# Performance work log

Measured on AMD Instinct MI355X. Metric: run time of the kernel, lower is better.

The kernel has to match this reference:

```python
import jax, jax.numpy as jnp
import numpy as np

B, T, V, D, H, L = 64, 256, 65, 384, 6, 6
HD = D // H
FF = 4 * D
EPS = 1e-5


def _layernorm(x, w, b):
    m = x.mean(-1, keepdims=True)
    v = ((x - m) ** 2).mean(-1, keepdims=True)
    return (x - m) / jnp.sqrt(v + EPS) * w + b


def setup_inputs() -> dict:
    key = jax.random.key(0)
    ks = jax.random.split(key, 20)
    s = lambda k, shape, scale=0.02: jax.random.normal(k, shape, dtype=jnp.float32) * scale
    inp = {
        'idx': jax.random.randint(ks[0], (B, T), 0, V),
        'tok_emb': s(ks[1], (V, D)),
        'pos_emb': s(ks[2], (T, D)),
        'ln1_w': jnp.ones((L, D), jnp.float32),
        'ln1_b': jnp.zeros((L, D), jnp.float32),
        'wq': s(ks[3], (L, H, D, HD)),
        'wk': s(ks[4], (L, H, D, HD)),
        'wv': s(ks[5], (L, H, D, HD)),
        'proj_w': s(ks[6], (L, D, D)),
        'proj_b': jnp.zeros((L, D), jnp.float32),
        'ln2_w': jnp.ones((L, D), jnp.float32),
        'ln2_b': jnp.zeros((L, D), jnp.float32),
        'ff_w1': s(ks[7], (L, D, FF)),
        'ff_b1': jnp.zeros((L, FF), jnp.float32),
        'ff_w2': s(ks[8], (L, FF, D)),
        'ff_b2': jnp.zeros((L, D), jnp.float32),
        'lnf_w': jnp.ones((D,), jnp.float32),
        'lnf_b': jnp.zeros((D,), jnp.float32),
        'head_w': s(ks[9], (D, V)),
        'head_b': jnp.zeros((V,), jnp.float32),
    }
    return inp


def reference(idx, tok_emb, pos_emb, ln1_w, ln1_b, wq, wk, wv, proj_w, proj_b,
              ln2_w, ln2_b, ff_w1, ff_b1, ff_w2, ff_b2, lnf_w, lnf_b, head_w, head_b):
    t = idx.shape[1]
    x = tok_emb[idx] + pos_emb[:t]  # [B,T,D]
    causal = jnp.tril(jnp.ones((t, t), bool))
    scale = D ** -0.5  # NOTE: original scales by n_embd**-0.5, not head_size
    for l in range(L):
        h = _layernorm(x, ln1_w[l], ln1_b[l])
        q = jnp.einsum('btd,hde->bhte', h, wq[l])
        k = jnp.einsum('btd,hde->bhte', h, wk[l])
        v = jnp.einsum('btd,hde->bhte', h, wv[l])
        wei = jnp.einsum('bhte,bhse->bhts', q, k) * scale
        wei = jnp.where(causal, wei, -jnp.inf)
        wei = jax.nn.softmax(wei, axis=-1)
        o = jnp.einsum('bhts,bhse->bhte', wei, v)
        o = o.transpose(0, 2, 1, 3).reshape(x.shape[0], t, D)  # concat heads
        x = x + o @ proj_w[l] + proj_b[l]
        h2 = _layernorm(x, ln2_w[l], ln2_b[l])
        x = x + jnp.maximum(h2 @ ff_w1[l] + ff_b1[l], 0.0) @ ff_w2[l] + ff_b2[l]
    x = _layernorm(x, lnf_w, lnf_b)
    logits = x @ head_w + head_b  # [B,T,V]
    return logits
```

## Files before the change

### kernel.cpp

```cpp
#include <hip/hip_runtime.h>
#include <hip/hip_bf16.h>
#include <math.h>

#define BB   64
#define TT   256
#define VV   65
#define DD   384
#define HH   6
#define HDD  64
#define LL   6
#define FFD  1536
#define BT   (BB * TT)
#define EPSL 1e-5f
#define SCALE 0.05103103630798287f

using bf16x8 = __attribute__((ext_vector_type(8))) short;
using f32x4  = __attribute__((ext_vector_type(4))) float;

__device__ __forceinline__ short f2bf(float f) {
    __hip_bfloat16 h = __float2bfloat16(f);
    return *reinterpret_cast<short*>(&h);
}

__device__ __forceinline__ void load_lds16(const void* g, void* lds_base) {
    __builtin_amdgcn_global_load_lds(
        (const __attribute__((address_space(1))) void*)g,
        (__attribute__((address_space(3))) void*)lds_base,
        16, 0, 0);
}

__global__ __launch_bounds__(256) void embed_k(const int* __restrict__ idx,
                                               const float* __restrict__ tok,
                                               const float* __restrict__ pos,
                                               float* __restrict__ x) {
    int i = blockIdx.x * 256 + threadIdx.x;
    int bt = i / 96;
    int d4 = i - bt * 96;
    int t  = bt & (TT - 1);
    float4 a = ((const float4*)tok)[(size_t)idx[bt] * 96 + d4];
    float4 p = ((const float4*)pos)[(size_t)t * 96 + d4];
    float4 o;
    o.x = a.x + p.x; o.y = a.y + p.y; o.z = a.z + p.z; o.w = a.w + p.w;
    ((float4*)x)[i] = o;
}

__global__ __launch_bounds__(256) void ln_k(const float* __restrict__ in,
                                            const float* __restrict__ w,
                                            const float* __restrict__ b,
                                            short* __restrict__ out) {
    int row  = blockIdx.x * 4 + (threadIdx.x >> 6);
    int lane = threadIdx.x & 63;
    const float* p = in + (size_t)row * DD;
    float vals[6];
    float s = 0.f;
#pragma unroll
    for (int j = 0; j < 6; ++j) { vals[j] = p[lane + 64 * j]; s += vals[j]; }
#pragma unroll
    for (int off = 32; off; off >>= 1) s += __shfl_xor(s, off);
    float mean = s * (1.0f / DD);
    float s2 = 0.f;
#pragma unroll
    for (int j = 0; j < 6; ++j) { float d = vals[j] - mean; s2 += d * d; }
#pragma unroll
    for (int off = 32; off; off >>= 1) s2 += __shfl_xor(s2, off);
    float rstd = rsqrtf(s2 * (1.0f / DD) + EPSL);
    short* po = out + (size_t)row * DD;
#pragma unroll
    for (int j = 0; j < 6; ++j) {
        int c = lane + 64 * j;
        po[c] = f2bf((vals[j] - mean) * rstd * w[c] + b[c]);
    }
}

__global__ __launch_bounds__(256) void wconv_k(const float* __restrict__ W,
                                               short* __restrict__ Wt,
                                               int K, int N, int Npad) {
    __shared__ float tile[32][33];
    W  += (size_t)blockIdx.z * K * N;
    Wt += (size_t)blockIdx.z * Npad * K;
    const int t  = threadIdx.x;
    const int c  = t & 31;
    const int r8 = t >> 5;
    const int k0 = blockIdx.y * 32;
    const int n0 = blockIdx.x * 32;
#pragma unroll
    for (int p = 0; p < 4; ++p) {
        int kk = r8 + 8 * p;
        int n  = n0 + c;
        tile[kk][c] = (n < N) ? W[(size_t)(k0 + kk) * N + n] : 0.f;
    }
    __syncthreads();
#pragma unroll
    for (int p = 0; p < 4; ++p) {
        int nl = r8 + 8 * p;
        Wt[(size_t)(n0 + nl) * K + k0 + c] = f2bf(tile[c][nl]);
    }
}

__global__ __launch_bounds__(256) void qkvconv_k(const float* __restrict__ wq,
                                                 const float* __restrict__ wk,
                                                 const float* __restrict__ wv,
                                                 short* __restrict__ Wt) {
    int tid = blockIdx.x * 256 + threadIdx.x;
    int e  = tid & 63;
    int k  = (tid >> 6) % 384;
    int r2 = (tid >> 6) / 384;
    int h  = r2 % 6;
    int r3 = r2 / 6;
    int part = r3 % 3;
    int l  = r3 / 3;
    const float* src = (part == 0) ? wq : (part == 1) ? wk : wv;
    float v = src[(((size_t)l * 6 + h) * 384 + k) * 64 + e];
    Wt[((size_t)l * 1152 + part * 384 + h * 64 + e) * 384 + k] = f2bf(v);
}

__global__ __launch_bounds__(256, 8) void gemm64_k(
    const short* __restrict__ A,
    const short* __restrict__ Bt,
    const float* __restrict__ bias,
    const float* __restrict__ res,
    float* __restrict__ out32,
    short* __restrict__ out16,
    int M, int K, int ldC, int ld16, int Nmax, int relu) {
    __shared__ short As[4096];
    __shared__ short Bs[4096];
    const int t  = threadIdx.x;
    const int w  = t >> 6;
    const int l  = t & 63;

    const int gx  = gridDim.x;
    const int nwg = gx * gridDim.y;
    const int lin = blockIdx.y * gx + blockIdx.x;
    const int cpx = nwg >> 3;
    const int swz = (lin & 7) * cpx + (lin >> 3);
    const int m0 = (swz / gx) * 64;
    const int n0 = (swz % gx) * 64;

    const int wr = w >> 1, wc = w & 1;
    const int fr = l & 15, fq = l >> 4;

    int srow[2], scol[2];
#pragma unroll
    for (int qi = 0; qi < 2; ++qi) {
        int s = w * 2 + qi;
        int r = s * 8 + (l >> 3);
        int c = l & 7;
        srow[qi] = r;
        scol[qi] = c ^ (r & 7);
    }

    f32x4 acc[2][2];
#pragma unroll
    for (int i = 0; i < 2; ++i)
#pragma unroll
        for (int j = 0; j < 2; ++j) acc[i][j] = (f32x4)(0.0f);

    const int nt = K >> 6;

    for (int tk = 0; tk < nt; ++tk) {
        const int k0 = tk << 6;
#pragma unroll
        for (int qi = 0; qi < 2; ++qi) {
            load_lds16(A + (size_t)(m0 + srow[qi]) * K + k0 + scol[qi] * 8,
                       (char*)As + (w * 2 + qi) * 1024);
        }
#pragma unroll
        for (int qi = 0; qi < 2; ++qi) {
            load_lds16(Bt + (size_t)(n0 + srow[qi]) * K + k0 + scol[qi] * 8,
                       (char*)Bs + (w * 2 + qi) * 1024);
        }
        asm volatile("s_waitcnt vmcnt(0)" ::: "memory");
        __syncthreads();

        __builtin_amdgcn_s_setprio(1);
#pragma unroll
        for (int ks = 0; ks < 2; ++ks) {
            const int kc = ks * 4 + fq;
            bf16x8 af[2], bfv[2];
#pragma unroll
            for (int mf = 0; mf < 2; ++mf) {
                int ar = wr * 32 + mf * 16 + fr;
                af[mf] = *reinterpret_cast<const bf16x8*>(
                    (const char*)As + ar * 128 + ((kc ^ (ar & 7)) << 4));
            }
#pragma unroll
            for (int nf = 0; nf < 2; ++nf) {
                int br = wc * 32 + nf * 16 + fr;
                bfv[nf] = *reinterpret_cast<const bf16x8*>(
                    (const char*)Bs + br * 128 + ((kc ^ (br & 7)) << 4));
            }
#pragma unroll
            for (int mf = 0; mf < 2; ++mf)
#pragma unroll
                for (int nf = 0; nf < 2; ++nf)
                    acc[mf][nf] = __builtin_amdgcn_mfma_f32_16x16x32_bf16(
                        af[mf], bfv[nf], acc[mf][nf], 0, 0, 0);
        }
        __builtin_amdgcn_s_setprio(0);
        __syncthreads();
    }

#pragma unroll
    for (int mf = 0; mf < 2; ++mf) {
#pragma unroll
        for (int nf = 0; nf < 2; ++nf) {
            int n = n0 + wc * 32 + nf * 16 + fr;
            if (n < Nmax) {
#pragma unroll
                for (int j = 0; j < 4; ++j) {
                    int m = m0 + wr * 32 + mf * 16 + fq * 4 + j;
                    float v = acc[mf][nf][j];
                    if (bias)  v += bias[n];
                    if (res)   v += res[(size_t)m * ldC + n];
                    if (relu)  v = fmaxf(v, 0.f);
                    if (out32) out32[(size_t)m * ldC + n] = v;
                    if (out16) out16[(size_t)m * ld16 + n] = f2bf(v);
                }
            }
        }
    }
}

__global__ __launch_bounds__(256) void attn_mfma_k(const short* __restrict__ qkv,
                                                   short* __restrict__ o) {
    __shared__ short Vt[16384];
    __shared__ short Pw[4][4096];

    const int hh = blockIdx.x;
    const int bb = blockIdx.y;
    const int t  = threadIdx.x;
    const int w  = t >> 6;
    const int lane = t & 63;
    const int fr = lane & 15, fq = lane >> 4;
    const int bt0 = bb * TT;

    {
        const int r0 = (t & 127) * 2;
        const int dbase = (t >> 7) * 32;
        const short* v0 = qkv + (size_t)(bt0 + r0) * 1152 + 768 + hh * 64 + dbase;
        short a0[32], a1[32];
#pragma unroll
        for (int i = 0; i < 4; ++i) {
            *(bf16x8*)(a0 + i * 8) = *(const bf16x8*)(v0 + i * 8);
            *(bf16x8*)(a1 + i * 8) = *(const bf16x8*)(v0 + 1152 + i * 8);
        }
#pragma unroll
        for (int i = 0; i < 32; ++i) {
            int d = dbase + i;
            int byte = (d * 512 + r0 * 2) ^ ((d & 7) << 4);
            unsigned int pk = (unsigned int)(unsigned short)a0[i] |
                              ((unsigned int)(unsigned short)a1[i] << 16);
            *(unsigned int*)((char*)Vt + byte) = pk;
        }
    }
    __syncthreads();

    char* PwW = (char*)Pw[w];

    bf16x8 qb[4][2];
#pragma unroll
    for (int nf = 0; nf < 4; ++nf)
#pragma unroll
        for (int ks = 0; ks < 2; ++ks)
            qb[nf][ks] = *(const bf16x8*)(qkv + (size_t)(bt0 + w * 64 + nf * 16 + fr) * 1152 +
                                          hh * 64 + ks * 32 + fq * 8);

    f32x4 o_acc[4][4];
#pragma unroll
    for (int i = 0; i < 4; ++i)
#pragma unroll
        for (int j = 0; j < 4; ++j) o_acc[i][j] = (f32x4)(0.0f);
    float m_run[4], l_run[4];
#pragma unroll
    for (int nf = 0; nf < 4; ++nf) { m_run[nf] = -1e30f; l_run[nf] = 0.f; }

    for (int kt = 0; kt <= w; ++kt) {
        bf16x8 ak[4][2];
#pragma unroll
        for (int mf = 0; mf < 4; ++mf)
#pragma unroll
            for (int ks = 0; ks < 2; ++ks)
                ak[mf][ks] = *(const bf16x8*)(qkv + (size_t)(bt0 + kt * 64 + mf * 16 + fr) * 1152 +
                                              384 + hh * 64 + ks * 32 + fq * 8);

        f32x4 s[4][4];
#pragma unroll
        for (int i = 0; i < 4; ++i)
#pragma unroll
            for (int j = 0; j < 4; ++j) s[i][j] = (f32x4)(0.0f);
#pragma unroll
        for (int ks = 0; ks < 2; ++ks)
#pragma unroll
            for (int mf = 0; mf < 4; ++mf)
#pragma unroll
                for (int nf = 0; nf < 4; ++nf)
                    s[mf][nf] = __builtin_amdgcn_mfma_f32_16x16x32_bf16(
                        ak[mf][ks], qb[nf][ks], s[mf][nf], 0, 0, 0);

        const bool diag = (kt == w);
#pragma unroll
        for (int mf = 0; mf < 4; ++mf)
#pragma unroll
            for (int nf = 0; nf < 4; ++nf)
#pragma unroll
                for (int j = 0; j < 4; ++j) {
                    float v = s[mf][nf][j] * SCALE;
                    if (diag && (mf * 16 + fq * 4 + j > nf * 16 + fr)) v = -1e30f;
                    s[mf][nf][j] = v;
                }

        float fac[4];
#pragma unroll
        for (int nf = 0; nf < 4; ++nf) {
            float mx = -1e30f;
#pragma unroll
            for (int mf = 0; mf < 4; ++mf)
#pragma unroll
                for (int j = 0; j < 4; ++j) mx = fmaxf(mx, s[mf][nf][j]);
            mx = fmaxf(mx, __shfl_xor(mx, 16));
            mx = fmaxf(mx, __shfl_xor(mx, 32));
            float mnew = fmaxf(m_run[nf], mx);
            fac[nf] = __expf(m_run[nf] - mnew);
            m_run[nf] = mnew;
        }

#pragma unroll
        for (int nf = 0; nf < 4; ++nf) {
            float ps = 0.f;
#pragma unroll
            for (int mf = 0; mf < 4; ++mf)
#pragma unroll
                for (int j = 0; j < 4; ++j) {
                    float p = __expf(s[mf][nf][j] - m_run[nf]);
                    s[mf][nf][j] = p;
                    ps += p;
                }
            ps += __shfl_xor(ps, 16);
            ps += __shfl_xor(ps, 32);
            l_run[nf] = l_run[nf] * fac[nf] + ps;
        }

#pragma unroll
        for (int mf = 0; mf < 4; ++mf)
#pragma unroll
            for (int nf = 0; nf < 4; ++nf) {
                unsigned long long pk =
                    (unsigned long long)(unsigned short)f2bf(s[mf][nf][0]) |
                    ((unsigned long long)(unsigned short)f2bf(s[mf][nf][1]) << 16) |
                    ((unsigned long long)(unsigned short)f2bf(s[mf][nf][2]) << 32) |
                    ((unsigned long long)(unsigned short)f2bf(s[mf][nf][3]) << 48);
                int q = nf * 16 + fr;
                int byte = (q * 128 + mf * 32 + fq * 8) ^ ((q & 7) << 4);
                *(unsigned long long*)(PwW + byte) = pk;
            }

#pragma unroll
        for (int j = 0; j < 4; ++j) {
            int src = (lane & 48) + ((lane & 48) >> 2) + j;
#pragma unroll
            for (int mo = 0; mo < 4; ++mo) {
                float f = __shfl(fac[mo], src);
#pragma unroll
                for (int df = 0; df < 4; ++df) o_acc[mo][df][j] *= f;
            }
        }

        bf16x8 ap[4][2], bv[4][2];
#pragma unroll
        for (int mo = 0; mo < 4; ++mo)
#pragma unroll
            for (int ks = 0; ks < 2; ++ks) {
                int byte = ((mo * 16 + fr) * 128 + ks * 64 + fq * 16) ^ ((fr & 7) << 4);
                ap[mo][ks] = *(const bf16x8*)(PwW + byte);
            }
#pragma unroll
        for (int df = 0; df < 4; ++df)
#pragma unroll
            for (int ks = 0; ks < 2; ++ks) {
                int byte = ((df * 16 + fr) * 512 + kt * 128 + ks * 64 + fq * 16) ^ ((fr & 7) << 4);
                bv[df][ks] = *(const bf16x8*)((const char*)Vt + byte);
            }
#pragma unroll
        for (int ks = 0; ks < 2; ++ks)
#pragma unroll
            for (int mo = 0; mo < 4; ++mo)
#pragma unroll
                for (int df = 0; df < 4; ++df)
                    o_acc[mo][df] = __builtin_amdgcn_mfma_f32_16x16x32_bf16(
                        ap[mo][ks], bv[df][ks], o_acc[mo][df], 0, 0, 0);
    }

    float linv[4];
#pragma unroll
    for (int nf = 0; nf < 4; ++nf) linv[nf] = 1.0f / l_run[nf];
#pragma unroll
    for (int j = 0; j < 4; ++j) {
        int src = (lane & 48) + ((lane & 48) >> 2) + j;
#pragma unroll
        for (int mo = 0; mo < 4; ++mo) {
            float li = __shfl(linv[mo], src);
#pragma unroll
            for (int df = 0; df < 4; ++df) {
                float val = o_acc[mo][df][j] * li;
                o[(size_t)(bt0 + w * 64 + mo * 16 + fq * 4 + j) * DD + hh * 64 + df * 16 + fr] =
                    f2bf(val);
            }
        }
    }
}

extern "C" void kernel_launch(void* const* d_in, const int* in_sizes, int n_in,
                              void* d_out, int out_size, void* d_ws, size_t ws_size,
                              hipStream_t stream) {
    const int*   idx     = (const int*)d_in[0];
    const float* tok_emb = (const float*)d_in[1];
    const float* pos_emb = (const float*)d_in[2];
    const float* ln1_w   = (const float*)d_in[3];
    const float* ln1_b   = (const float*)d_in[4];
    const float* wq      = (const float*)d_in[5];
    const float* wk      = (const float*)d_in[6];
    const float* wv      = (const float*)d_in[7];
    const float* proj_w  = (const float*)d_in[8];
    const float* proj_b  = (const float*)d_in[9];
    const float* ln2_w   = (const float*)d_in[10];
    const float* ln2_b   = (const float*)d_in[11];
    const float* ff_w1   = (const float*)d_in[12];
    const float* ff_b1   = (const float*)d_in[13];
    const float* ff_w2   = (const float*)d_in[14];
    const float* ff_b2   = (const float*)d_in[15];
    const float* lnf_w   = (const float*)d_in[16];
    const float* lnf_b   = (const float*)d_in[17];
    const float* head_w  = (const float*)d_in[18];
    const float* head_b  = (const float*)d_in[19];
    float* out = (float*)d_out;

    char* p = (char*)d_ws;
    float* x      = (float*)p;  p += (size_t)BT * DD * 4;
    short* qkv16  = (short*)p;  p += (size_t)BT * 1152 * 2;
    short* h16    = (short*)p;  p += (size_t)BT * DD * 2;
    short* o16    = (short*)p;  p += (size_t)BT * DD * 2;
    short* ff16   = (short*)p;  p += (size_t)BT * FFD * 2;
    short* wqkvT  = (short*)p;  p += (size_t)LL * 1152 * 384 * 2;
    short* projT  = (short*)p;  p += (size_t)LL * 384 * 384 * 2;
    short* ff1T   = (short*)p;  p += (size_t)LL * 1536 * 384 * 2;
    short* ff2T   = (short*)p;  p += (size_t)LL * 384 * 1536 * 2;
    short* headT  = (short*)p;  p += (size_t)128 * 384 * 2;

    const dim3 blk(256);

    qkvconv_k<<<dim3(2654208 / 256), blk, 0, stream>>>(wq, wk, wv, wqkvT);
    wconv_k<<<dim3(12, 12, 6), blk, 0, stream>>>(proj_w, projT, 384, 384, 384);
    wconv_k<<<dim3(48, 12, 6), blk, 0, stream>>>(ff_w1, ff1T, 384, 1536, 1536);
    wconv_k<<<dim3(12, 48, 6), blk, 0, stream>>>(ff_w2, ff2T, 1536, 384, 384);
    wconv_k<<<dim3(4, 12, 1), blk, 0, stream>>>(head_w, headT, 384, 65, 128);

    embed_k<<<dim3((BT * 96) / 256), blk, 0, stream>>>(idx, tok_emb, pos_emb, x);

    const dim3 gLN(BT / 4);
    const dim3 gAttn(HH, BB);
    const dim3 gQKV(1152 / 64, BT / 64);
    const dim3 gD(384 / 64, BT / 64);
    const dim3 gFF(1536 / 64, BT / 64);
    const dim3 gHead(128 / 64, BT / 64);

    for (int l = 0; l < LL; ++l) {
        const size_t dOff = (size_t)l * DD;

        ln_k<<<gLN, blk, 0, stream>>>(x, ln1_w + dOff, ln1_b + dOff, h16);

        gemm64_k<<<gQKV, blk, 0, stream>>>(h16, wqkvT + (size_t)l * 1152 * 384,
                                           nullptr, nullptr, nullptr, qkv16,
                                           BT, 384, 1152, 1152, 1152, 0);

        attn_mfma_k<<<gAttn, blk, 0, stream>>>(qkv16, o16);

        gemm64_k<<<gD, blk, 0, stream>>>(o16, projT + (size_t)l * 384 * 384,
                                         proj_b + dOff, x, x, nullptr,
                                         BT, 384, 384, 0, 384, 0);

        ln_k<<<gLN, blk, 0, stream>>>(x, ln2_w + dOff, ln2_b + dOff, h16);

        gemm64_k<<<gFF, blk, 0, stream>>>(h16, ff1T + (size_t)l * 1536 * 384,
                                          ff_b1 + (size_t)l * FFD, nullptr,
                                          nullptr, ff16,
                                          BT, 384, 1536, 1536, 1536, 1);

        gemm64_k<<<gD, blk, 0, stream>>>(ff16, ff2T + (size_t)l * 384 * 1536,
                                         ff_b2 + dOff, x, x, nullptr,
                                         BT, 1536, 384, 0, 384, 0);
    }

    ln_k<<<gLN, blk, 0, stream>>>(x, lnf_w, lnf_b, h16);
    gemm64_k<<<gHead, blk, 0, stream>>>(h16, headT, head_b, nullptr, out, nullptr,
                                        BT, 384, 65, 0, 65, 0);
}
```

Before: 1.195 ms.

## Store residual stream in bf16 and enlarge GEMM tiles to 128x64

The residual activation x is now kept in bf16 instead of fp32: embedding, layernorm input and the GEMM residual epilogue all read and write bf16, which halves that memory traffic. The GEMM kernel moves from 64x64 to 128x64 output tiles with 4x2 MFMA fragments per wave, so each B tile is reused more and fewer blocks are launched. The cost is that the residual accumulates rounding error in bf16 across layers, plus higher register and LDS use per block, which lowers occupancy.

```diff
diff --git a/kernel.cpp b/kernel.cpp
--- a/kernel.cpp
+++ b/kernel.cpp
@@ -21,6 +21,11 @@
     __hip_bfloat16 h = __float2bfloat16(f);
     return *reinterpret_cast<short*>(&h);
 }
+__device__ __forceinline__ float bf2f(short s) {
+    union { unsigned u; float f; } c;
+    c.u = ((unsigned)(unsigned short)s) << 16;
+    return c.f;
+}
 
 __device__ __forceinline__ void load_lds16(const void* g, void* lds_base) {
     __builtin_amdgcn_global_load_lds(
@@ -32,44 +37,52 @@
 __global__ __launch_bounds__(256) void embed_k(const int* __restrict__ idx,
                                                const float* __restrict__ tok,
                                                const float* __restrict__ pos,
-                                               float* __restrict__ x) {
+                                               short* __restrict__ x) {
     int i = blockIdx.x * 256 + threadIdx.x;
-    int bt = i / 96;
-    int d4 = i - bt * 96;
+    int bt = i / 48;
+    int g  = i - bt * 48;
     int t  = bt & (TT - 1);
-    float4 a = ((const float4*)tok)[(size_t)idx[bt] * 96 + d4];
-    float4 p = ((const float4*)pos)[(size_t)t * 96 + d4];
-    float4 o;
-    o.x = a.x + p.x; o.y = a.y + p.y; o.z = a.z + p.z; o.w = a.w + p.w;
-    ((float4*)x)[i] = o;
-}
-
-__global__ __launch_bounds__(256) void ln_k(const float* __restrict__ in,
+    const float4* tp = (const float4*)tok + (size_t)idx[bt] * 96 + g * 2;
+    const float4* pp = (const float4*)pos + (size_t)t * 96 + g * 2;
+    float4 a0 = tp[0], a1 = tp[1], p0 = pp[0], p1 = pp[1];
+    bf16x8 o;
+    o[0] = f2bf(a0.x + p0.x); o[1] = f2bf(a0.y + p0.y);
+    o[2] = f2bf(a0.z + p0.z); o[3] = f2bf(a0.w + p0.w);
+    o[4] = f2bf(a1.x + p1.x); o[5] = f2bf(a1.y + p1.y);
+    o[6] = f2bf(a1.z + p1.z); o[7] = f2bf(a1.w + p1.w);
+    *reinterpret_cast<bf16x8*>(x + (size_t)bt * DD + g * 8) = o;
+}
+
+__global__ __launch_bounds__(256) void ln_k(const short* __restrict__ in,
                                             const float* __restrict__ w,
                                             const float* __restrict__ b,
                                             short* __restrict__ out) {
     int row  = blockIdx.x * 4 + (threadIdx.x >> 6);
     int lane = threadIdx.x & 63;
-    const float* p = in + (size_t)row * DD;
-    float vals[6];
-    float s = 0.f;
-#pragma unroll
-    for (int j = 0; j < 6; ++j) { vals[j] = p[lane + 64 * j]; s += vals[j]; }
+    const unsigned* pu = (const unsigned*)(in + (size_t)row * DD);
+    unsigned u0 = pu[lane], u1 = pu[lane + 64], u2 = pu[lane + 128];
+    float v00 = bf2f((short)(u0 & 0xffff)), v01 = bf2f((short)(u0 >> 16));
+    float v10 = bf2f((short)(u1 & 0xffff)), v11 = bf2f((short)(u1 >> 16));
+    float v20 = bf2f((short)(u2 & 0xffff)), v21 = bf2f((short)(u2 >> 16));
+    float s = v00 + v01 + v10 + v11 + v20 + v21;
 #pragma unroll
     for (int off = 32; off; off >>= 1) s += __shfl_xor(s, off);
     float mean = s * (1.0f / DD);
-    float s2 = 0.f;
-#pragma unroll
-    for (int j = 0; j < 6; ++j) { float d = vals[j] - mean; s2 += d * d; }
+    float d00 = v00 - mean, d01 = v01 - mean, d10 = v10 - mean,
+          d11 = v11 - mean, d20 = v20 - mean, d21 = v21 - mean;
+    float s2 = d00*d00 + d01*d01 + d10*d10 + d11*d11 + d20*d20 + d21*d21;
 #pragma unroll
     for (int off = 32; off; off >>= 1) s2 += __shfl_xor(s2, off);
     float rstd = rsqrtf(s2 * (1.0f / DD) + EPSL);
-    short* po = out + (size_t)row * DD;
-#pragma unroll
-    for (int j = 0; j < 6; ++j) {
-        int c = lane + 64 * j;
-        po[c] = f2bf((vals[j] - mean) * rstd * w[c] + b[c]);
-    }
+    int c0 = lane * 2, c1 = c0 + 128, c2 = c0 + 256;
+    unsigned* po = (unsigned*)(out + (size_t)row * DD);
+    unsigned r0 = (unsigned)(unsigned short)f2bf(d00 * rstd * w[c0] + b[c0]) |
+                  ((unsigned)(unsigned short)f2bf(d01 * rstd * w[c0+1] + b[c0+1]) << 16);
+    unsigned r1 = (unsigned)(unsigned short)f2bf(d10 * rstd * w[c1] + b[c1]) |
+                  ((unsigned)(unsigned short)f2bf(d11 * rstd * w[c1+1] + b[c1+1]) << 16);
+    unsigned r2 = (unsigned)(unsigned short)f2bf(d20 * rstd * w[c2] + b[c2]) |
+                  ((unsigned)(unsigned short)f2bf(d21 * rstd * w[c2+1] + b[c2+1]) << 16);
+    po[lane] = r0; po[lane + 64] = r1; po[lane + 128] = r2;
 }
 
 __global__ __launch_bounds__(256) void wconv_k(const float* __restrict__ W,
@@ -114,16 +127,16 @@
     Wt[((size_t)l * 1152 + part * 384 + h * 64 + e) * 384 + k] = f2bf(v);
 }
 
-__global__ __launch_bounds__(256, 8) void gemm64_k(
+__global__ __launch_bounds__(256, 6) void gemm128_k(
     const short* __restrict__ A,
     const short* __restrict__ Bt,
     const float* __restrict__ bias,
-    const float* __restrict__ res,
+    const short* __restrict__ res16,
     float* __restrict__ out32,
     short* __restrict__ out16,
-    int M, int K, int ldC, int ld16, int Nmax, int relu) {
-    __shared__ short As[4096];
-    __shared__ short Bs[4096];
+    int M, int K, int ldC, int Nmax, int relu) {
+    __shared__ short As[128 * 64];
+    __shared__ short Bs[64 * 64];
     const int t  = threadIdx.x;
     const int w  = t >> 6;
     const int l  = t & 63;
@@ -133,25 +146,30 @@
     const int lin = blockIdx.y * gx + blockIdx.x;
     const int cpx = nwg >> 3;
     const int swz = (lin & 7) * cpx + (lin >> 3);
-    const int m0 = (swz / gx) * 64;
+    const int m0 = (swz / gx) * 128;
     const int n0 = (swz % gx) * 64;
 
     const int wr = w >> 1, wc = w & 1;
     const int fr = l & 15, fq = l >> 4;
 
-    int srow[2], scol[2];
+    int arow[4], acol[4];
+#pragma unroll
+    for (int qi = 0; qi < 4; ++qi) {
+        int r = (w * 4 + qi) * 8 + (l >> 3);
+        arow[qi] = r;
+        acol[qi] = (l & 7) ^ (r & 7);
+    }
+    int brow[2], bcol[2];
 #pragma unroll
     for (int qi = 0; qi < 2; ++qi) {
-        int s = w * 2 + qi;
-        int r = s * 8 + (l >> 3);
-        int c = l & 7;
-        srow[qi] = r;
-        scol[qi] = c ^ (r & 7);
-    }
-
-    f32x4 acc[2][2];
-#pragma unroll
-    for (int i = 0; i < 2; ++i)
+        int r = (w * 2 + qi) * 8 + (l >> 3);
+        brow[qi] = r;
+        bcol[qi] = (l & 7) ^ (r & 7);
+    }
+
+    f32x4 acc[4][2];
+#pragma unroll
+    for (int i = 0; i < 4; ++i)
 #pragma unroll
         for (int j = 0; j < 2; ++j) acc[i][j] = (f32x4)(0.0f);
 
@@ -160,15 +178,13 @@
     for (int tk = 0; tk < nt; ++tk) {
         const int k0 = tk << 6;
 #pragma unroll
-        for (int qi = 0; qi < 2; ++qi) {
-            load_lds16(A + (size_t)(m0 + srow[qi]) * K + k0 + scol[qi] * 8,
-                       (char*)As + (w * 2 + qi) * 1024);
-        }
-#pragma unroll
-        for (int qi = 0; qi < 2; ++qi) {
-            load_lds16(Bt + (size_t)(n0 + srow[qi]) * K + k0 + scol[qi] * 8,
+        for (int qi = 0; qi < 4; ++qi)
+            load_lds16(A + (size_t)(m0 + arow[qi]) * K + k0 + acol[qi] * 8,
+                       (char*)As + (w * 4 + qi) * 1024);
+#pragma unroll
+        for (int qi = 0; qi < 2; ++qi)
+            load_lds16(Bt + (size_t)(n0 + brow[qi]) * K + k0 + bcol[qi] * 8,
                        (char*)Bs + (w * 2 + qi) * 1024);
-        }
         asm volatile("s_waitcnt vmcnt(0)" ::: "memory");
         __syncthreads();
 
@@ -176,10 +192,10 @@
 #pragma unroll
         for (int ks = 0; ks < 2; ++ks) {
             const int kc = ks * 4 + fq;
-            bf16x8 af[2], bfv[2];
-#pragma unroll
-            for (int mf = 0; mf < 2; ++mf) {
-                int ar = wr * 32 + mf * 16 + fr;
+            bf16x8 af[4], bfv[2];
+#pragma unroll
+            for (int mf = 0; mf < 4; ++mf) {
+                int ar = wr * 64 + mf * 16 + fr;
                 af[mf] = *reinterpret_cast<const bf16x8*>(
                     (const char*)As + ar * 128 + ((kc ^ (ar & 7)) << 4));
             }
@@ -190,7 +206,7 @@
                     (const char*)Bs + br * 128 + ((kc ^ (br & 7)) << 4));
             }
 #pragma unroll
-            for (int mf = 0; mf < 2; ++mf)
+            for (int mf = 0; mf < 4; ++mf)
 #pragma unroll
                 for (int nf = 0; nf < 2; ++nf)
                     acc[mf][nf] = __builtin_amdgcn_mfma_f32_16x16x32_bf16(
@@ -201,20 +217,20 @@
     }
 
 #pragma unroll
-    for (int mf = 0; mf < 2; ++mf) {
+    for (int mf = 0; mf < 4; ++mf) {
 #pragma unroll
         for (int nf = 0; nf < 2; ++nf) {
             int n = n0 + wc * 32 + nf * 16 + fr;
             if (n < Nmax) {
 #pragma unroll
                 for (int j = 0; j < 4; ++j) {
-                    int m = m0 + wr * 32 + mf * 16 + fq * 4 + j;
+                    int m = m0 + wr * 64 + mf * 16 + fq * 4 + j;
                     float v = acc[mf][nf][j];
-                    if (bias)  v += bias[n];
-                    if (res)   v += res[(size_t)m * ldC + n];
-                    if (relu)  v = fmaxf(v, 0.f);
-                    if (out32) out32[(size_t)m * ldC + n] = v;
-                    if (out16) out16[(size_t)m * ld16 + n] = f2bf(v);
+                    if (bias)   v += bias[n];
+                    if (res16)  v += bf2f(res16[(size_t)m * ldC + n]);
+                    if (relu)   v = fmaxf(v, 0.f);
+                    if (out32)  out32[(size_t)m * ldC + n] = v;
+                    if (out16)  out16[(size_t)m * ldC + n] = f2bf(v);
                 }
             }
         }
@@ -435,7 +451,7 @@
     float* out = (float*)d_out;
 
     char* p = (char*)d_ws;
-    float* x      = (float*)p;  p += (size_t)BT * DD * 4;
+    short* x16    = (short*)p;  p += (size_t)BT * DD * 2;
     short* qkv16  = (short*)p;  p += (size_t)BT * 1152 * 2;
     short* h16    = (short*)p;  p += (size_t)BT * DD * 2;
     short* o16    = (short*)p;  p += (size_t)BT * DD * 2;
@@ -454,43 +470,43 @@
     wconv_k<<<dim3(12, 48, 6), blk, 0, stream>>>(ff_w2, ff2T, 1536, 384, 384);
     wconv_k<<<dim3(4, 12, 1), blk, 0, stream>>>(head_w, headT, 384, 65, 128);
 
-    embed_k<<<dim3((BT * 96) / 256), blk, 0, stream>>>(idx, tok_emb, pos_emb, x);
+    embed_k<<<dim3((BT * 48) / 256), blk, 0, stream>>>(idx, tok_emb, pos_emb, x16);
 
     const dim3 gLN(BT / 4);
     const dim3 gAttn(HH, BB);
-    const dim3 gQKV(1152 / 64, BT / 64);
-    const dim3 gD(384 / 64, BT / 64);
-    const dim3 gFF(1536 / 64, BT / 64);
-    const dim3 gHead(128 / 64, BT / 64);
+    const dim3 gQKV(1152 / 64, BT / 128);
+    const dim3 gD(384 / 64, BT / 128);
+    const dim3 gFF(1536 / 64, BT / 128);
+    const dim3 gHead(128 / 64, BT / 128);
 
     for (int l = 0; l < LL; ++l) {
         const size_t dOff = (size_t)l * DD;
 
-        ln_k<<<gLN, blk, 0, stream>>>(x, ln1_w + dOff, ln1_b + dOff, h16);
-
-        gemm64_k<<<gQKV, blk, 0, stream>>>(h16, wqkvT + (size_t)l * 1152 * 384,
-                                           nullptr, nullptr, nullptr, qkv16,
-                                           BT, 384, 1152, 1152, 1152, 0);
+        ln_k<<<gLN, blk, 0, stream>>>(x16, ln1_w + dOff, ln1_b + dOff, h16);
+
+        gemm128_k<<<gQKV, blk, 0, stream>>>(h16, wqkvT + (size_t)l * 1152 * 384,
+                                            nullptr, nullptr, nullptr, qkv16,
+                                            BT, 384, 1152, 1152, 0);
 
         attn_mfma_k<<<gAttn, blk, 0, stream>>>(qkv16, o16);
 
-        gemm64_k<<<gD, blk, 0, stream>>>(o16, projT + (size_t)l * 384 * 384,
-                                         proj_b + dOff, x, x, nullptr,
-                                         BT, 384, 384, 0, 384, 0);
-
-        ln_k<<<gLN, blk, 0, stream>>>(x, ln2_w + dOff, ln2_b + dOff, h16);
-
-        gemm64_k<<<gFF, blk, 0, stream>>>(h16, ff1T + (size_t)l * 1536 * 384,
-                                          ff_b1 + (size_t)l * FFD, nullptr,
-                                          nullptr, ff16,
-                                          BT, 384, 1536, 1536, 1536, 1);
-
-        gemm64_k<<<gD, blk, 0, stream>>>(ff16, ff2T + (size_t)l * 384 * 1536,
-                                         ff_b2 + dOff, x, x, nullptr,
-                                         BT, 1536, 384, 0, 384, 0);
-    }
-
-    ln_k<<<gLN, blk, 0, stream>>>(x, lnf_w, lnf_b, h16);
-    gemm64_k<<<gHead, blk, 0, stream>>>(h16, headT, head_b, nullptr, out, nullptr,
-                                        BT, 384, 65, 0, 65, 0);
-}
+        gemm128_k<<<gD, blk, 0, stream>>>(o16, projT + (size_t)l * 384 * 384,
+                                          proj_b + dOff, x16, nullptr, x16,
+                                          BT, 384, 384, 384, 0);
+
+        ln_k<<<gLN, blk, 0, stream>>>(x16, ln2_w + dOff, ln2_b + dOff, h16);
+
+        gemm128_k<<<gFF, blk, 0, stream>>>(h16, ff1T + (size_t)l * 1536 * 384,
+                                           ff_b1 + (size_t)l * FFD, nullptr,
+                                           nullptr, ff16,
+                                           BT, 384, 1536, 1536, 1);
+
+        gemm128_k<<<gD, blk, 0, stream>>>(ff16, ff2T + (size_t)l * 384 * 1536,
+                                          ff_b2 + dOff, x16, nullptr, x16,
+                                          BT, 1536, 384, 384, 0);
+    }
+
+    ln_k<<<gLN, blk, 0, stream>>>(x16, lnf_w, lnf_b, h16);
+    gemm128_k<<<gHead, blk, 0, stream>>>(h16, headT, head_b, nullptr, out, nullptr,
+                                         BT, 384, 65, 65, 0);
+}
```

After: 1.287 ms. 1.08x slower.
